# Kernel tuning notes

Measured on AMD Instinct MI355X. Metric: run time of the kernel, lower is better.

The kernel has to match this reference:

```python
import jax, jax.numpy as jnp
import numpy as np

B, H, W = 8, 512, 512
KSIZE = 11   # HVS Gaussian kernel size
SIGMA = 2.0
EPS = 1e-8


def _gauss_kernel():
    ax = jnp.arange(KSIZE, dtype=jnp.float32) - (KSIZE - 1) / 2.0
    g = jnp.exp(-(ax ** 2) / (2.0 * SIGMA ** 2))
    k = jnp.outer(g, g)
    return k / jnp.sum(k)


def _conv_same(x, k):
    # x: (B,1,H,W), k: (kh,kw) symmetric -> conv == correlation
    return jax.lax.conv_general_dilated(
        x, k[None, None, :, :], window_strides=(1, 1), padding='SAME',
        dimension_numbers=('NCHW', 'OIHW', 'NCHW'))


def setup_inputs() -> dict:
    key = jax.random.key(0)
    k1, k2, k3 = jax.random.split(key, 3)
    prob_map = jax.random.uniform(k1, (B, 1, H, W), dtype=jnp.float32,
                                  minval=0.01, maxval=0.99)
    c = jax.random.uniform(k2, (B, 1, H, W), dtype=jnp.float32)
    # binary halftone sampled per-pixel from prob_map
    h_sampled = (jax.random.uniform(k3, (B, 1, H, W)) < prob_map).astype(jnp.float32)
    return {"prob_map": prob_map, "c": c, "h_sampled": h_sampled}


def reference(prob_map, c, h_sampled):
    k = _gauss_kernel()
    # perceived error of the sampled halftone: e = G*h - c
    e = _conv_same(h_sampled, k) - c                     # (B,1,H,W)
    corr = _conv_same(e, k)                              # (G*e), G symmetric
    sum_k2 = jnp.sum(k * k)
    delta = 1.0 - 2.0 * h_sampled                        # flip change per pixel
    # reward_calc.compute_reward_with_flip, vectorized over all pixels:
    # E(flip at a) - E = 2*delta_a*(G*e)(a) + delta_a^2 * sum(G^2)
    reward = 2.0 * delta * corr + (delta ** 2) * sum_k2  # >0 means flip hurts
    log_prob = jnp.where(h_sampled > 0.5,
                         jnp.log(prob_map + EPS),
                         jnp.log(1.0 - prob_map + EPS))
    # local expected-gradient (REINFORCE) loss, averaged over batch
    loss = -jnp.sum(reward * log_prob) / prob_map.shape[0]
    return loss
```

## Files before the change

kernel.cpp:

```cpp
#include <hip/hip_runtime.h>

typedef float v2f __attribute__((ext_vector_type(2)));
typedef float v4f __attribute__((ext_vector_type(4)));

#define IMG 512
#define NBLK 1024

#define A_STR  92
#define BT_STR 46
#define ET_STR 44
#define CT_STR 36

__device__ __forceinline__ v2f lo2(v4f v) { return __builtin_shufflevector(v, v, 0, 1); }
__device__ __forceinline__ v2f hi2(v4f v) { return __builtin_shufflevector(v, v, 2, 3); }

__device__ __forceinline__ v4f ldq(const float* __restrict__ hmap, size_t base,
                                   int x0, int y0, int idx) {
    int r = idx / 22, q = idx - r * 22;
    int gy = y0 - 10 + r, gx0 = x0 - 12 + 4 * q;
    v4f v = {0.f, 0.f, 0.f, 0.f};
    if ((unsigned)gy < IMG) {
        const float* hr = &hmap[base + ((size_t)gy << 9)];
        if (gx0 >= 0 && gx0 + 3 < IMG) {
            v = *(const v4f*)&hr[gx0];
        } else {
            if ((unsigned)(gx0 + 0) < IMG) v.x = hr[gx0 + 0];
            if ((unsigned)(gx0 + 1) < IMG) v.y = hr[gx0 + 1];
            if ((unsigned)(gx0 + 2) < IMG) v.z = hr[gx0 + 2];
            if ((unsigned)(gx0 + 3) < IMG) v.w = hr[gx0 + 3];
        }
    }
    return v;
}

__global__ __launch_bounds__(256, 4) void marl_fused(
    const float* __restrict__ prob,
    const float* __restrict__ cmap,
    const float* __restrict__ hmap,
    float* __restrict__ ws)
{
    __shared__ __align__(16) float Abuf[52 * A_STR];
    __shared__ __align__(16) float Bbuf[88 * BT_STR];
    __shared__ float red[4];

    const float W[11] = {0.00881223f, 0.02714358f, 0.06511405f, 0.12164908f,
                         0.17699840f, 0.20056540f, 0.17699840f, 0.12164908f,
                         0.06511405f, 0.02714358f, 0.00881223f};
    v2f wv[11];
#pragma unroll
    for (int i = 0; i < 11; ++i) wv[i] = (v2f){W[i], W[i]};
    float w2 = 0.f;
#pragma unroll
    for (int i = 0; i < 11; ++i) w2 += W[i] * W[i];
    const float sumk2 = w2 * w2;
    const v2f z = {0.f, 0.f};

    const int tid = threadIdx.x;
    const int T  = blockIdx.x;
    const int b  = T >> 7, r7 = T & 127;
    const int x0 = (r7 & 7) << 6, y0 = (r7 >> 3) << 5;
    const size_t base = (size_t)b << 18;

    const int p1run = tid % 7, p1q = tid / 7;
    const int p2p = tid % 21, p2exo = tid / 21;
    const int p3ex = tid >> 1, p3oy0 = (tid & 1) << 4;
    const int ox0 = (tid >> 4) << 2, oy0e = (tid & 15) << 1;

    float creg[2][8];
    v4f hq[2], pq[2];
    {
        v4f s0 = ldq(hmap, base, x0, y0, tid);
        v4f s1 = ldq(hmap, base, x0, y0, tid + 256);
        v4f s2 = ldq(hmap, base, x0, y0, tid + 512);
        v4f s3 = ldq(hmap, base, x0, y0, tid + 768);
        v4f s4 = (tid < 120) ? ldq(hmap, base, x0, y0, tid + 1024) : (v4f){0.f,0.f,0.f,0.f};
        if (tid < 210) {
#pragma unroll
            for (int h = 0; h < 2; ++h) {
                int gy = y0 - 5 + 2 * p2p + h;
#pragma unroll
                for (int c = 0; c < 8; ++c) {
                    int gx = x0 - 5 + 8 * p2exo + c;
                    creg[h][c] = ((unsigned)gy < IMG && (unsigned)gx < IMG)
                        ? cmap[base + ((size_t)gy << 9) + gx] : 0.f;
                }
            }
        }
#pragma unroll
        for (int h = 0; h < 2; ++h) {
            size_t rowb = base + ((size_t)(y0 + oy0e + h) << 9) + (x0 + ox0);
            hq[h] = *(const v4f*)&hmap[rowb];
            pq[h] = *(const v4f*)&prob[rowb];
        }
        { int i = tid;       int r = i / 22, q = i - r * 22; *(v4f*)&Abuf[r * A_STR + 4 * q] = s0; }
        { int i = tid + 256; int r = i / 22, q = i - r * 22; *(v4f*)&Abuf[r * A_STR + 4 * q] = s1; }
        { int i = tid + 512; int r = i / 22, q = i - r * 22; *(v4f*)&Abuf[r * A_STR + 4 * q] = s2; }
        { int i = tid + 768; int r = i / 22, q = i - r * 22; *(v4f*)&Abuf[r * A_STR + 4 * q] = s3; }
        if (tid < 120) { int i = tid + 1024; int r = i / 22, q = i - r * 22;
                         *(v4f*)&Abuf[r * A_STR + 4 * q] = s4; }
    }
    __syncthreads();

    if (tid < 154) {
        int by0 = 6 * p1run;
        v2f accLo[6] = {z, z, z, z, z, z}, accHi[6] = {z, z, z, z, z, z};
#pragma unroll
        for (int i = 0; i < 16; ++i) {
            v4f a = *(const v4f*)&Abuf[(by0 + i) * A_STR + 4 * p1q];
            v2f lo = lo2(a), hi = hi2(a);
#pragma unroll
            for (int r = 0; r < 6; ++r) {
                int j = i - r;
                if (j >= 0 && j < 11) { accLo[r] += wv[j] * lo; accHi[r] += wv[j] * hi; }
            }
        }
#pragma unroll
        for (int r = 0; r < 6; ++r) {
            int by = by0 + r;
            Bbuf[(4 * p1q + 0) * BT_STR + by] = accLo[r].x;
            Bbuf[(4 * p1q + 1) * BT_STR + by] = accLo[r].y;
            Bbuf[(4 * p1q + 2) * BT_STR + by] = accHi[r].x;
            Bbuf[(4 * p1q + 3) * BT_STR + by] = accHi[r].y;
        }
    }
    __syncthreads();

    if (tid < 210) {
        int ex0 = 8 * p2exo, ey0 = 2 * p2p;
        v2f acc[8] = {z, z, z, z, z, z, z, z};
#pragma unroll
        for (int i = 0; i < 18; ++i) {
            int cb = ex0 + 2 + i; cb = cb > 85 ? 85 : cb;
            v2f bb = *(const v2f*)&Bbuf[cb * BT_STR + ey0];
#pragma unroll
            for (int c = 0; c < 8; ++c) {
                int j = i - c;
                if (j >= 0 && j < 11) acc[c] += wv[j] * bb;
            }
        }
#pragma unroll
        for (int c = 0; c < 8; ++c) {
            int ex = ex0 + c;
            if (ex < 74) {
                int gx = x0 - 5 + ex;
                bool xin = (unsigned)gx < IMG;
                v2f ev;
#pragma unroll
                for (int h = 0; h < 2; ++h) {
                    int gy = y0 - 5 + ey0 + h;
                    ev[h] = (xin && (unsigned)gy < IMG) ? acc[c][h] - creg[h][c] : 0.f;
                }
                *(v2f*)&Abuf[ex * ET_STR + ey0] = ev;
            }
        }
    }
    __syncthreads();

    if (tid < 148) {
        const float* src = &Abuf[p3ex * ET_STR + p3oy0];
        float win[26];
#pragma unroll
        for (int k = 0; k < 6; ++k)
            *(v4f*)&win[4 * k] = *(const v4f*)&src[4 * k];
        *(v2f*)&win[24] = *(const v2f*)&src[24];
        float o[16];
#pragma unroll
        for (int k = 0; k < 16; ++k) {
            float acc = 0.f;
#pragma unroll
            for (int j = 0; j < 11; ++j) acc += W[j] * win[k + j];
            o[k] = acc;
        }
#pragma unroll
        for (int k = 0; k < 4; ++k)
            *(v4f*)&Bbuf[p3ex * CT_STR + p3oy0 + 4 * k] =
                (v4f){o[4 * k], o[4 * k + 1], o[4 * k + 2], o[4 * k + 3]};
    }
    __syncthreads();

    float partial = 0.f;
    {
        v2f acc[4] = {z, z, z, z};
#pragma unroll
        for (int i = 0; i < 14; ++i) {
            v2f ct = *(const v2f*)&Bbuf[(ox0 + i) * CT_STR + oy0e];
#pragma unroll
            for (int c = 0; c < 4; ++c) {
                int j = i - c;
                if (j >= 0 && j < 11) acc[c] += wv[j] * ct;
            }
        }
#pragma unroll
        for (int h = 0; h < 2; ++h) {
#pragma unroll
            for (int c = 0; c < 4; ++c) {
                float h_ = hq[h][c], p_ = pq[h][c];
                float logp = __logf(h_ > 0.5f ? p_ + 1e-8f : 1.f - p_ + 1e-8f);
                float delta = 1.f - 2.f * h_;
                partial += (2.f * delta * acc[c][h] + sumk2) * logp;
            }
        }
    }

#pragma unroll
    for (int off = 32; off > 0; off >>= 1)
        partial += __shfl_down(partial, off, 64);
    if ((tid & 63) == 0) red[tid >> 6] = partial;
    __syncthreads();
    if (tid == 0)
        ws[blockIdx.x] = red[0] + red[1] + red[2] + red[3];
}

__global__ __launch_bounds__(256) void marl_reduce(const float* __restrict__ ws,
                                                   float* __restrict__ out)
{
    __shared__ float red[4];
    const int tid = threadIdx.x;
    float s = ws[tid] + ws[tid + 256] + ws[tid + 512] + ws[tid + 768];
#pragma unroll
    for (int off = 32; off > 0; off >>= 1)
        s += __shfl_down(s, off, 64);
    if ((tid & 63) == 0) red[tid >> 6] = s;
    __syncthreads();
    if (tid == 0)
        out[0] = -0.125f * (red[0] + red[1] + red[2] + red[3]);
}

extern "C" void kernel_launch(void* const* d_in, const int* in_sizes, int n_in,
                              void* d_out, int out_size, void* d_ws, size_t ws_size,
                              hipStream_t stream) {
    const float* prob = (const float*)d_in[0];
    const float* cmap = (const float*)d_in[1];
    const float* hmap = (const float*)d_in[2];
    float* out = (float*)d_out;
    float* ws  = (float*)d_ws;

    marl_fused<<<dim3(NBLK), dim3(256), 0, stream>>>(prob, cmap, hmap, ws);
    marl_reduce<<<dim3(1), dim3(256), 0, stream>>>(ws, out);
}
```

Measured before the change: 83.15 us.

## Enlarge tiles to 64x64 per block to cut halo overhead

Each block now covers a 64x64 output tile instead of 64x32, halving the block count to 512. All four separable convolution passes and the shared-memory buffers are re-partitioned for the larger tile, and each thread now handles more outputs. The aim is to shrink the fraction of redundant halo loads and halo computation in the doubled-convolution pipeline. In exchange it uses more shared memory and registers (occupancy hint lowered to 2 blocks per CU), and 512 blocks may under-fill the GPU.

Measured after the change: 85.04 us. 2.3% more time.

```diff
diff --git a/kernel.cpp b/kernel.cpp
--- a/kernel.cpp
+++ b/kernel.cpp
@@ -4,12 +4,12 @@
 typedef float v4f __attribute__((ext_vector_type(4)));
 
 #define IMG 512
-#define NBLK 1024
+#define NBLK 512
 
 #define A_STR  92
-#define BT_STR 46
-#define ET_STR 44
-#define CT_STR 36
+#define BT_STR 74
+#define ET_STR 76
+#define CT_STR 68
 
 __device__ __forceinline__ v2f lo2(v4f v) { return __builtin_shufflevector(v, v, 0, 1); }
 __device__ __forceinline__ v2f hi2(v4f v) { return __builtin_shufflevector(v, v, 2, 3); }
@@ -33,13 +33,13 @@
     return v;
 }
 
-__global__ __launch_bounds__(256, 4) void marl_fused(
+__global__ __launch_bounds__(256, 2) void marl_fused(
     const float* __restrict__ prob,
     const float* __restrict__ cmap,
     const float* __restrict__ hmap,
     float* __restrict__ ws)
 {
-    __shared__ __align__(16) float Abuf[52 * A_STR];
+    __shared__ __align__(16) float Abuf[84 * A_STR];
     __shared__ __align__(16) float Bbuf[88 * BT_STR];
     __shared__ float red[4];
 
@@ -57,89 +57,98 @@
 
     const int tid = threadIdx.x;
     const int T  = blockIdx.x;
-    const int b  = T >> 7, r7 = T & 127;
-    const int x0 = (r7 & 7) << 6, y0 = (r7 >> 3) << 5;
+    const int b  = T >> 6, r6 = T & 63;
+    const int x0 = (r6 & 7) << 6, y0 = (r6 >> 3) << 6;
     const size_t base = (size_t)b << 18;
 
-    const int p1run = tid % 7, p1q = tid / 7;
-    const int p2p = tid % 21, p2exo = tid / 21;
-    const int p3ex = tid >> 1, p3oy0 = (tid & 1) << 4;
-    const int ox0 = (tid >> 4) << 2, oy0e = (tid & 15) << 1;
-
-    float creg[2][8];
-    v4f hq[2], pq[2];
+    const int p1run = tid % 11, p1q = tid / 11;
+    const int p2p = tid % 37, p2g = tid / 37;
+    const int ox0 = (tid >> 5) << 3, oy0e = (tid & 31) << 1;
+
+    float creg[2][16];
+    v4f hqa[2], hqb[2], pqa[2], pqb[2];
     {
-        v4f s0 = ldq(hmap, base, x0, y0, tid);
-        v4f s1 = ldq(hmap, base, x0, y0, tid + 256);
-        v4f s2 = ldq(hmap, base, x0, y0, tid + 512);
-        v4f s3 = ldq(hmap, base, x0, y0, tid + 768);
-        v4f s4 = (tid < 120) ? ldq(hmap, base, x0, y0, tid + 1024) : (v4f){0.f,0.f,0.f,0.f};
-        if (tid < 210) {
+        v4f st[8];
+#pragma unroll
+        for (int k = 0; k < 7; ++k) st[k] = ldq(hmap, base, x0, y0, tid + 256 * k);
+        st[7] = (tid < 56) ? ldq(hmap, base, x0, y0, tid + 1792) : (v4f){0.f,0.f,0.f,0.f};
+        if (tid < 185) {
 #pragma unroll
             for (int h = 0; h < 2; ++h) {
                 int gy = y0 - 5 + 2 * p2p + h;
-#pragma unroll
-                for (int c = 0; c < 8; ++c) {
-                    int gx = x0 - 5 + 8 * p2exo + c;
-                    creg[h][c] = ((unsigned)gy < IMG && (unsigned)gx < IMG)
-                        ? cmap[base + ((size_t)gy << 9) + gx] : 0.f;
+                bool yin = (unsigned)gy < IMG;
+                const float* cr = &cmap[base + ((size_t)gy << 9)];
+#pragma unroll
+                for (int c = 0; c < 16; ++c) {
+                    int gx = x0 - 5 + 16 * p2g + c;
+                    creg[h][c] = (yin && (unsigned)gx < IMG) ? cr[gx] : 0.f;
                 }
             }
         }
 #pragma unroll
         for (int h = 0; h < 2; ++h) {
             size_t rowb = base + ((size_t)(y0 + oy0e + h) << 9) + (x0 + ox0);
-            hq[h] = *(const v4f*)&hmap[rowb];
-            pq[h] = *(const v4f*)&prob[rowb];
-        }
-        { int i = tid;       int r = i / 22, q = i - r * 22; *(v4f*)&Abuf[r * A_STR + 4 * q] = s0; }
-        { int i = tid + 256; int r = i / 22, q = i - r * 22; *(v4f*)&Abuf[r * A_STR + 4 * q] = s1; }
-        { int i = tid + 512; int r = i / 22, q = i - r * 22; *(v4f*)&Abuf[r * A_STR + 4 * q] = s2; }
-        { int i = tid + 768; int r = i / 22, q = i - r * 22; *(v4f*)&Abuf[r * A_STR + 4 * q] = s3; }
-        if (tid < 120) { int i = tid + 1024; int r = i / 22, q = i - r * 22;
-                         *(v4f*)&Abuf[r * A_STR + 4 * q] = s4; }
-    }
-    __syncthreads();
-
-    if (tid < 154) {
-        int by0 = 6 * p1run;
-        v2f accLo[6] = {z, z, z, z, z, z}, accHi[6] = {z, z, z, z, z, z};
-#pragma unroll
-        for (int i = 0; i < 16; ++i) {
-            v4f a = *(const v4f*)&Abuf[(by0 + i) * A_STR + 4 * p1q];
+            hqa[h] = *(const v4f*)&hmap[rowb];
+            hqb[h] = *(const v4f*)&hmap[rowb + 4];
+            pqa[h] = *(const v4f*)&prob[rowb];
+            pqb[h] = *(const v4f*)&prob[rowb + 4];
+        }
+#pragma unroll
+        for (int k = 0; k < 7; ++k) {
+            int idx = tid + 256 * k;
+            int r = idx / 22, q = idx - r * 22;
+            *(v4f*)&Abuf[r * A_STR + 4 * q] = st[k];
+        }
+        if (tid < 56) {
+            int idx = tid + 1792;
+            int r = idx / 22, q = idx - r * 22;
+            *(v4f*)&Abuf[r * A_STR + 4 * q] = st[7];
+        }
+    }
+    __syncthreads();
+
+    if (tid < 242) {
+        int by0 = 7 * p1run;
+        v2f accLo[7] = {z, z, z, z, z, z, z}, accHi[7] = {z, z, z, z, z, z, z};
+#pragma unroll
+        for (int i = 0; i < 17; ++i) {
+            int rr = by0 + i; rr = rr > 83 ? 83 : rr;
+            v4f a = *(const v4f*)&Abuf[rr * A_STR + 4 * p1q];
             v2f lo = lo2(a), hi = hi2(a);
 #pragma unroll
-            for (int r = 0; r < 6; ++r) {
+            for (int r = 0; r < 7; ++r) {
                 int j = i - r;
                 if (j >= 0 && j < 11) { accLo[r] += wv[j] * lo; accHi[r] += wv[j] * hi; }
             }
         }
 #pragma unroll
-        for (int r = 0; r < 6; ++r) {
+        for (int r = 0; r < 7; ++r) {
             int by = by0 + r;
-            Bbuf[(4 * p1q + 0) * BT_STR + by] = accLo[r].x;
-            Bbuf[(4 * p1q + 1) * BT_STR + by] = accLo[r].y;
-            Bbuf[(4 * p1q + 2) * BT_STR + by] = accHi[r].x;
-            Bbuf[(4 * p1q + 3) * BT_STR + by] = accHi[r].y;
-        }
-    }
-    __syncthreads();
-
-    if (tid < 210) {
-        int ex0 = 8 * p2exo, ey0 = 2 * p2p;
-        v2f acc[8] = {z, z, z, z, z, z, z, z};
-#pragma unroll
-        for (int i = 0; i < 18; ++i) {
-            int cb = ex0 + 2 + i; cb = cb > 85 ? 85 : cb;
+            if (by < 74) {
+                Bbuf[(4 * p1q + 0) * BT_STR + by] = accLo[r].x;
+                Bbuf[(4 * p1q + 1) * BT_STR + by] = accLo[r].y;
+                Bbuf[(4 * p1q + 2) * BT_STR + by] = accHi[r].x;
+                Bbuf[(4 * p1q + 3) * BT_STR + by] = accHi[r].y;
+            }
+        }
+    }
+    __syncthreads();
+
+    if (tid < 185) {
+        int ex0 = 16 * p2g, ey0 = 2 * p2p;
+        v2f acc[16] = {z, z, z, z, z, z, z, z, z, z, z, z, z, z, z, z};
+#pragma unroll
+        for (int i = 0; i < 26; ++i) {
+            int cb = ex0 + 2 + i; cb = cb > 87 ? 87 : cb;
             v2f bb = *(const v2f*)&Bbuf[cb * BT_STR + ey0];
 #pragma unroll
-            for (int c = 0; c < 8; ++c) {
+            for (int c = 0; c < 16; ++c) {
                 int j = i - c;
                 if (j >= 0 && j < 11) acc[c] += wv[j] * bb;
             }
         }
 #pragma unroll
-        for (int c = 0; c < 8; ++c) {
+        for (int c = 0; c < 16; ++c) {
             int ex = ex0 + c;
             if (ex < 74) {
                 int gx = x0 - 5 + ex;
@@ -156,8 +165,11 @@
     }
     __syncthreads();
 
-    if (tid < 148) {
-        const float* src = &Abuf[p3ex * ET_STR + p3oy0];
+#pragma unroll
+    for (int w = tid; w < 296; w += 256) {
+        int wex = w % 74, woyq = w / 74;
+        int oy0 = 16 * woyq;
+        const float* src = &Abuf[wex * ET_STR + oy0];
         float win[26];
 #pragma unroll
         for (int k = 0; k < 6; ++k)
@@ -173,19 +185,19 @@
         }
 #pragma unroll
         for (int k = 0; k < 4; ++k)
-            *(v4f*)&Bbuf[p3ex * CT_STR + p3oy0 + 4 * k] =
+            *(v4f*)&Bbuf[wex * CT_STR + oy0 + 4 * k] =
                 (v4f){o[4 * k], o[4 * k + 1], o[4 * k + 2], o[4 * k + 3]};
     }
     __syncthreads();
 
     float partial = 0.f;
     {
-        v2f acc[4] = {z, z, z, z};
-#pragma unroll
-        for (int i = 0; i < 14; ++i) {
+        v2f acc[8] = {z, z, z, z, z, z, z, z};
+#pragma unroll
+        for (int i = 0; i < 18; ++i) {
             v2f ct = *(const v2f*)&Bbuf[(ox0 + i) * CT_STR + oy0e];
 #pragma unroll
-            for (int c = 0; c < 4; ++c) {
+            for (int c = 0; c < 8; ++c) {
                 int j = i - c;
                 if (j >= 0 && j < 11) acc[c] += wv[j] * ct;
             }
@@ -193,8 +205,9 @@
 #pragma unroll
         for (int h = 0; h < 2; ++h) {
 #pragma unroll
-            for (int c = 0; c < 4; ++c) {
-                float h_ = hq[h][c], p_ = pq[h][c];
+            for (int c = 0; c < 8; ++c) {
+                float h_ = (c < 4) ? hqa[h][c] : hqb[h][c - 4];
+                float p_ = (c < 4) ? pqa[h][c] : pqb[h][c - 4];
                 float logp = __logf(h_ > 0.5f ? p_ + 1e-8f : 1.f - p_ + 1e-8f);
                 float delta = 1.f - 2.f * h_;
                 partial += (2.f * delta * acc[c][h] + sumk2) * logp;
@@ -216,7 +229,7 @@
 {
     __shared__ float red[4];
     const int tid = threadIdx.x;
-    float s = ws[tid] + ws[tid + 256] + ws[tid + 512] + ws[tid + 768];
+    float s = ws[tid] + ws[tid + 256];
 #pragma unroll
     for (int off = 32; off > 0; off >>= 1)
         s += __shfl_down(s, off, 64);
```
